# Optimization experiments

Hardware: AMD Instinct MI355X
Metric: run time of the kernel (lower is better)

## Reference

```python
import jax, jax.numpy as jnp
import numpy as np

B, S, D, H = 8, 1024, 1024, 16
DH = D // H


def setup_inputs() -> dict:
    key = jax.random.key(0)
    ks = jax.random.split(key, 8)
    x = jax.random.normal(ks[0], (B, S, D), dtype=jnp.float32)
    # Whisper-style additive causal mask: -inf above the diagonal
    mask = jnp.triu(jnp.full((S, S), -jnp.inf, dtype=jnp.float32), k=1)
    s = 0.02
    Wq = jax.random.normal(ks[1], (D, D), jnp.float32) * s
    bq = jax.random.normal(ks[2], (D,), jnp.float32) * s
    Wk = jax.random.normal(ks[3], (D, D), jnp.float32) * s
    Wv = jax.random.normal(ks[4], (D, D), jnp.float32) * s
    bv = jax.random.normal(ks[5], (D,), jnp.float32) * s
    Wo = jax.random.normal(ks[6], (D, D), jnp.float32) * s
    bo = jax.random.normal(ks[7], (D,), jnp.float32) * s
    return {"x": x, "mask": mask, "Wq": Wq, "bq": bq, "Wk": Wk, "Wv": Wv,
            "bv": bv, "Wo": Wo, "bo": bo}


def reference(x, mask, Wq, bq, Wk, Wv, bv, Wo, bo):
    n_head = H
    d_head = D // n_head
    scale = d_head ** -0.25

    # Projections (torch Linear: y = x @ W.T + b; key has no bias)
    q = x @ Wq.T + bq           # [B,S,D]
    k = x @ Wk.T                # [B,S,D]
    v = x @ Wv.T + bv           # [B,S,D]

    # [B,S,D] -> [B,H,S,dh]
    q = q.reshape(B, S, n_head, d_head).transpose(0, 2, 1, 3)
    k = k.reshape(B, S, n_head, d_head).transpose(0, 2, 1, 3)
    v = v.reshape(B, S, n_head, d_head).transpose(0, 2, 1, 3)

    # Manual (non-fused) attention, fp32 softmax, as in the torch path
    qk = jnp.einsum('bhqd,bhkd->bhqk', q * scale, k * scale)
    qk = qk + mask[:S, :S]
    qk = qk.astype(jnp.float32)
    w = jax.nn.softmax(qk, axis=-1).astype(q.dtype)
    out = jnp.einsum('bhqk,bhkd->bhqd', w, v)
    out = out.transpose(0, 2, 1, 3).reshape(B, S, D)
    out = out @ Wo.T + bo
    qk = jax.lax.stop_gradient(qk)
    return out, qk
```

## Files before the change

kernel.cpp:

```cpp
#include <hip/hip_runtime.h>
#include <math.h>

constexpr int B_ = 8, S_ = 1024, D_ = 1024, H_ = 16, DH_ = 64;
constexpr float MASK_NEG = -1e30f;

typedef __attribute__((ext_vector_type(8))) short short8;
typedef __attribute__((ext_vector_type(4))) float f32x4;

union S8U { short8 s8; unsigned u[4]; };

__device__ __forceinline__ void split8(float4 a, float4 b, short8* hi, short8* lo) {
  float f[8] = {a.x, a.y, a.z, a.w, b.x, b.y, b.z, b.w};
  S8U h, l;
#pragma unroll
  for (int i = 0; i < 4; ++i) {
    float p = f[2 * i], q = f[2 * i + 1];
    unsigned up = __float_as_uint(p), uq = __float_as_uint(q);
    unsigned hp = up & 0xFFFF0000u, hq = uq & 0xFFFF0000u;
    float lp = p - __uint_as_float(hp);
    float lq = q - __uint_as_float(hq);
    h.u[i] = hq | (hp >> 16);
    l.u[i] = (__float_as_uint(lq) & 0xFFFF0000u) | (__float_as_uint(lp) >> 16);
  }
  *hi = h.s8;
  *lo = l.s8;
}

__device__ __forceinline__ void split1v(float f, short& hi, short& lo) {
  unsigned u = __float_as_uint(f);
  unsigned hb = u & 0xFFFF0000u;
  float l = f - __uint_as_float(hb);
  hi = (short)(hb >> 16);
  lo = (short)(__float_as_uint(l) >> 16);
}

__device__ __forceinline__ unsigned pack_sp(float f) {
  unsigned u = __float_as_uint(f);
  unsigned hb = u & 0xFFFF0000u;
  float lo = f - __uint_as_float(hb);
  return hb | (__float_as_uint(lo) >> 16);
}

__device__ __forceinline__ void unpack8(uint4 a, uint4 b, short8* hi, short8* lo) {
  S8U h, l;
  h.u[0] = (a.y & 0xFFFF0000u) | (a.x >> 16);
  h.u[1] = (a.w & 0xFFFF0000u) | (a.z >> 16);
  h.u[2] = (b.y & 0xFFFF0000u) | (b.x >> 16);
  h.u[3] = (b.w & 0xFFFF0000u) | (b.z >> 16);
  l.u[0] = (a.y << 16) | (a.x & 0xFFFFu);
  l.u[1] = (a.w << 16) | (a.z & 0xFFFFu);
  l.u[2] = (b.y << 16) | (b.x & 0xFFFFu);
  l.u[3] = (b.w << 16) | (b.z & 0xFFFFu);
  *hi = h.s8;
  *lo = l.s8;
}

__global__ __launch_bounds__(256) void split_planes(
    const float* __restrict__ x, short* xh, short* xl,
    const float* __restrict__ w0, short* w0h, short* w0l,
    const float* __restrict__ w1, short* w1h, short* w1l,
    const float* __restrict__ w2, short* w2h, short* w2l,
    const float* __restrict__ w3, short* w3h, short* w3l) {
  const float* src; short *dh, *dl; int n8;
  switch (blockIdx.y) {
    case 0:  src = x;  dh = xh;  dl = xl;  n8 = (B_ * S_ * D_) / 8; break;
    case 1:  src = w0; dh = w0h; dl = w0l; n8 = (D_ * D_) / 8; break;
    case 2:  src = w1; dh = w1h; dl = w1l; n8 = (D_ * D_) / 8; break;
    case 3:  src = w2; dh = w2h; dl = w2l; n8 = (D_ * D_) / 8; break;
    default: src = w3; dh = w3h; dl = w3l; n8 = (D_ * D_) / 8; break;
  }
  for (int i = blockIdx.x * 256 + threadIdx.x; i < n8; i += gridDim.x * 256) {
    float4 a = ((const float4*)src)[2 * i];
    float4 b = ((const float4*)src)[2 * i + 1];
    short8 h, l;
    split8(a, b, &h, &l);
    ((short8*)dh)[i] = h;
    ((short8*)dl)[i] = l;
  }
}

__global__ __launch_bounds__(256) void gemm_planes(
    const short* __restrict__ Ah, const short* __restrict__ Al,
    const short* __restrict__ Wh, const short* __restrict__ Wl,
    const float* __restrict__ bias, float scale, int mode,
    float* __restrict__ C, short* __restrict__ Ch, short* __restrict__ Cl,
    int M, int N, int K) {
  __shared__ __align__(16) short As_h[128][40];
  __shared__ __align__(16) short As_l[128][40];
  __shared__ __align__(16) short Bs_h[128][40];
  __shared__ __align__(16) short Bs_l[128][40];

  const int tid = threadIdx.x;
  const int m0 = blockIdx.y * 128, n0 = blockIdx.x * 128;
  const int wave = tid >> 6, lane = tid & 63;
  const int wm = (wave & 1) * 64, wn = (wave >> 1) * 64;
  const int lm = lane & 15;
  const int koff = (lane >> 4) * 8;

  const int r0 = tid >> 2, r1 = (tid >> 2) + 64;
  const int u0 = (tid & 3) * 8;

  f32x4 acc[4][4];
#pragma unroll
  for (int i = 0; i < 4; ++i)
#pragma unroll
    for (int j = 0; j < 4; ++j) acc[i][j] = (f32x4){0.f, 0.f, 0.f, 0.f};

  for (int k0 = 0; k0 < K; k0 += 32) {
    __syncthreads();
    short8 t0 = *(const short8*)(Ah + (size_t)(m0 + r0) * K + k0 + u0);
    short8 t1 = *(const short8*)(Ah + (size_t)(m0 + r1) * K + k0 + u0);
    short8 t2 = *(const short8*)(Al + (size_t)(m0 + r0) * K + k0 + u0);
    short8 t3 = *(const short8*)(Al + (size_t)(m0 + r1) * K + k0 + u0);
    short8 t4 = *(const short8*)(Wh + (size_t)(n0 + r0) * K + k0 + u0);
    short8 t5 = *(const short8*)(Wh + (size_t)(n0 + r1) * K + k0 + u0);
    short8 t6 = *(const short8*)(Wl + (size_t)(n0 + r0) * K + k0 + u0);
    short8 t7 = *(const short8*)(Wl + (size_t)(n0 + r1) * K + k0 + u0);
    *(short8*)&As_h[r0][u0] = t0;
    *(short8*)&As_h[r1][u0] = t1;
    *(short8*)&As_l[r0][u0] = t2;
    *(short8*)&As_l[r1][u0] = t3;
    *(short8*)&Bs_h[r0][u0] = t4;
    *(short8*)&Bs_h[r1][u0] = t5;
    *(short8*)&Bs_l[r0][u0] = t6;
    *(short8*)&Bs_l[r1][u0] = t7;
    __syncthreads();

    short8 ah[4], al[4], bh[4], bl[4];
#pragma unroll
    for (int i = 0; i < 4; ++i) {
      ah[i] = *(const short8*)&As_h[wm + i * 16 + lm][koff];
      al[i] = *(const short8*)&As_l[wm + i * 16 + lm][koff];
      bh[i] = *(const short8*)&Bs_h[wn + i * 16 + lm][koff];
      bl[i] = *(const short8*)&Bs_l[wn + i * 16 + lm][koff];
    }
#pragma unroll
    for (int i = 0; i < 4; ++i)
#pragma unroll
      for (int j = 0; j < 4; ++j) {
        acc[i][j] = __builtin_amdgcn_mfma_f32_16x16x32_bf16(ah[i], bh[j], acc[i][j], 0, 0, 0);
        acc[i][j] = __builtin_amdgcn_mfma_f32_16x16x32_bf16(ah[i], bl[j], acc[i][j], 0, 0, 0);
        acc[i][j] = __builtin_amdgcn_mfma_f32_16x16x32_bf16(al[i], bh[j], acc[i][j], 0, 0, 0);
      }
  }

  const int crow0 = (lane >> 4) * 4;
  const int ccol = lane & 15;
#pragma unroll
  for (int i = 0; i < 4; ++i) {
    const int m = m0 + wm + i * 16 + crow0;
#pragma unroll
    for (int j = 0; j < 4; ++j) {
      const int n = n0 + wn + j * 16 + ccol;
      const float bv_ = bias ? bias[n] : 0.f;
      if (mode == 0) {
#pragma unroll
        for (int r = 0; r < 4; ++r)
          C[(size_t)(m + r) * N + n] = acc[i][j][r] + bv_;
      } else if (mode == 1) {
#pragma unroll
        for (int r = 0; r < 4; ++r) {
          float v = (acc[i][j][r] + bv_) * scale;
          short hv, lv;
          split1v(v, hv, lv);
          Ch[(size_t)(m + r) * N + n] = hv;
          Cl[(size_t)(m + r) * N + n] = lv;
        }
      } else {
        const int bb = m >> 10, ss = m & 1023;
        short4 hv, lv;
        split1v(acc[i][j][0] + bv_, hv.x, lv.x);
        split1v(acc[i][j][1] + bv_, hv.y, lv.y);
        split1v(acc[i][j][2] + bv_, hv.z, lv.z);
        split1v(acc[i][j][3] + bv_, hv.w, lv.w);
        *(short4*)(Ch + ((size_t)bb * D_ + n) * S_ + ss) = hv;
        *(short4*)(Cl + ((size_t)bb * D_ + n) * S_ + ss) = lv;
      }
    }
  }
}

__global__ __launch_bounds__(256) void attn_fused(
    const short* __restrict__ qsh, const short* __restrict__ qsl,
    const short* __restrict__ ksh, const short* __restrict__ ksl,
    const short* __restrict__ vsh, const short* __restrict__ vsl,
    float* __restrict__ qk, short* __restrict__ oh, short* __restrict__ ol) {
  __shared__ __align__(16) short K_hi[64][72];
  __shared__ __align__(16) short K_lo[64][72];
  __shared__ __align__(16) short V_hi[64][72];
  __shared__ __align__(16) short V_lo[64][72];
  __shared__ __align__(16) unsigned P_p[64][68];

  const int it = blockIdx.x;
  const int bh = blockIdx.y;
  const int b = bh >> 4, h = bh & 15;
  const int tid = threadIdx.x;
  const int wave = tid >> 6, lane = tid & 63;
  const int lm = lane & 15, lg = lane >> 4;
  const int wq = wave * 16;
  const int koff = lg * 8;
  const int crow0 = lg * 4;
  const int sr0 = tid >> 3, sr1 = (tid >> 3) + 32;
  const int sc0 = (tid & 7) * 8;

  short8 qfh[2], qfl[2];
  {
    const size_t qb = ((size_t)(b * S_ + it * 64 + wq + lm)) * D_ + h * DH_;
    qfh[0] = *(const short8*)(qsh + qb + koff);
    qfh[1] = *(const short8*)(qsh + qb + 32 + koff);
    qfl[0] = *(const short8*)(qsl + qb + koff);
    qfl[1] = *(const short8*)(qsl + qb + 32 + koff);
  }

  f32x4 O[4];
#pragma unroll
  for (int i = 0; i < 4; ++i) O[i] = (f32x4){0.f, 0.f, 0.f, 0.f};
  f32x4 mreg = (f32x4){MASK_NEG, MASK_NEG, MASK_NEG, MASK_NEG};
  f32x4 lreg = (f32x4){0.f, 0.f, 0.f, 0.f};

  float* qkrow = qk + ((size_t)bh << 20) + (size_t)it * 64 * S_;

  for (int jt = 0; jt <= it; ++jt) {
    __syncthreads();
    const size_t kb = ((size_t)(b * S_ + jt * 64)) * D_ + h * DH_;
    const size_t vb = ((size_t)(b * D_ + h * DH_)) * S_ + jt * 64;
    short8 a0 = *(const short8*)(ksh + kb + (size_t)sr0 * D_ + sc0);
    short8 a1 = *(const short8*)(ksh + kb + (size_t)sr1 * D_ + sc0);
    short8 a2 = *(const short8*)(ksl + kb + (size_t)sr0 * D_ + sc0);
    short8 a3 = *(const short8*)(ksl + kb + (size_t)sr1 * D_ + sc0);
    short8 a4 = *(const short8*)(vsh + vb + (size_t)sr0 * S_ + sc0);
    short8 a5 = *(const short8*)(vsh + vb + (size_t)sr1 * S_ + sc0);
    short8 a6 = *(const short8*)(vsl + vb + (size_t)sr0 * S_ + sc0);
    short8 a7 = *(const short8*)(vsl + vb + (size_t)sr1 * S_ + sc0);
    *(short8*)&K_hi[sr0][sc0] = a0;
    *(short8*)&K_hi[sr1][sc0] = a1;
    *(short8*)&K_lo[sr0][sc0] = a2;
    *(short8*)&K_lo[sr1][sc0] = a3;
    *(short8*)&V_hi[sr0][sc0] = a4;
    *(short8*)&V_hi[sr1][sc0] = a5;
    *(short8*)&V_lo[sr0][sc0] = a6;
    *(short8*)&V_lo[sr1][sc0] = a7;
    __syncthreads();

    f32x4 sacc[4];
#pragma unroll
    for (int j4 = 0; j4 < 4; ++j4) sacc[j4] = (f32x4){0.f, 0.f, 0.f, 0.f};
#pragma unroll
    for (int kc = 0; kc < 2; ++kc)
#pragma unroll
      for (int j4 = 0; j4 < 4; ++j4) {
        short8 kh = *(const short8*)&K_hi[j4 * 16 + lm][kc * 32 + koff];
        short8 kl = *(const short8*)&K_lo[j4 * 16 + lm][kc * 32 + koff];
        sacc[j4] = __builtin_amdgcn_mfma_f32_16x16x32_bf16(qfh[kc], kh, sacc[j4], 0, 0, 0);
        sacc[j4] = __builtin_amdgcn_mfma_f32_16x16x32_bf16(qfh[kc], kl, sacc[j4], 0, 0, 0);
        sacc[j4] = __builtin_amdgcn_mfma_f32_16x16x32_bf16(qfl[kc], kh, sacc[j4], 0, 0, 0);
      }

    if (jt == it) {
#pragma unroll
      for (int j4 = 0; j4 < 4; ++j4)
#pragma unroll
        for (int r = 0; r < 4; ++r)
          if (j4 * 16 + lm > wq + crow0 + r) sacc[j4][r] = MASK_NEG;
    }

#pragma unroll
    for (int j4 = 0; j4 < 4; ++j4)
#pragma unroll
      for (int r = 0; r < 4; ++r)
        qkrow[(size_t)(wq + crow0 + r) * S_ + jt * 64 + j4 * 16 + lm] = sacc[j4][r];

    f32x4 tmax = sacc[0];
#pragma unroll
    for (int j4 = 1; j4 < 4; ++j4)
#pragma unroll
      for (int r = 0; r < 4; ++r) tmax[r] = fmaxf(tmax[r], sacc[j4][r]);
#pragma unroll
    for (int off = 1; off < 16; off <<= 1)
#pragma unroll
      for (int r = 0; r < 4; ++r) tmax[r] = fmaxf(tmax[r], __shfl_xor(tmax[r], off));

    f32x4 fac, mnew;
#pragma unroll
    for (int r = 0; r < 4; ++r) {
      mnew[r] = fmaxf(mreg[r], tmax[r]);
      fac[r] = __expf(mreg[r] - mnew[r]);
      mreg[r] = mnew[r];
    }
    f32x4 tsum = (f32x4){0.f, 0.f, 0.f, 0.f};
#pragma unroll
    for (int j4 = 0; j4 < 4; ++j4)
#pragma unroll
      for (int r = 0; r < 4; ++r) {
        float pv = __expf(sacc[j4][r] - mnew[r]);
        sacc[j4][r] = pv;
        tsum[r] += pv;
      }
#pragma unroll
    for (int off = 1; off < 16; off <<= 1)
#pragma unroll
      for (int r = 0; r < 4; ++r) tsum[r] += __shfl_xor(tsum[r], off);
#pragma unroll
    for (int r = 0; r < 4; ++r) lreg[r] = lreg[r] * fac[r] + tsum[r];
#pragma unroll
    for (int d4 = 0; d4 < 4; ++d4)
#pragma unroll
      for (int r = 0; r < 4; ++r) O[d4][r] *= fac[r];

#pragma unroll
    for (int j4 = 0; j4 < 4; ++j4)
#pragma unroll
      for (int r = 0; r < 4; ++r)
        P_p[wq + crow0 + r][j4 * 16 + lm] = pack_sp(sacc[j4][r]);
    __syncthreads();

#pragma unroll
    for (int kc = 0; kc < 2; ++kc) {
      const unsigned* pp = &P_p[wq + lm][kc * 32 + koff];
      uint4 a0p = *(const uint4*)pp;
      uint4 a1p = *(const uint4*)(pp + 4);
      short8 ph, pl;
      unpack8(a0p, a1p, &ph, &pl);
#pragma unroll
      for (int d4 = 0; d4 < 4; ++d4) {
        short8 vh = *(const short8*)&V_hi[d4 * 16 + lm][kc * 32 + koff];
        short8 vl = *(const short8*)&V_lo[d4 * 16 + lm][kc * 32 + koff];
        O[d4] = __builtin_amdgcn_mfma_f32_16x16x32_bf16(ph, vh, O[d4], 0, 0, 0);
        O[d4] = __builtin_amdgcn_mfma_f32_16x16x32_bf16(ph, vl, O[d4], 0, 0, 0);
        O[d4] = __builtin_amdgcn_mfma_f32_16x16x32_bf16(pl, vh, O[d4], 0, 0, 0);
      }
    }
  }

  {
    f32x4 inv;
#pragma unroll
    for (int r = 0; r < 4; ++r) inv[r] = 1.f / lreg[r];
    const size_t ob = ((size_t)(b * S_ + it * 64 + wq + crow0)) * D_ + h * DH_;
#pragma unroll
    for (int d4 = 0; d4 < 4; ++d4)
#pragma unroll
      for (int r = 0; r < 4; ++r) {
        float v = O[d4][r] * inv[r];
        short hv, lv;
        split1v(v, hv, lv);
        oh[ob + (size_t)r * D_ + d4 * 16 + lm] = hv;
        ol[ob + (size_t)r * D_ + d4 * 16 + lm] = lv;
      }
  }

  const int fr = tid >> 4, fc = (tid & 15) * 4;
  const float4 nf = make_float4(MASK_NEG, MASK_NEG, MASK_NEG, MASK_NEG);
  for (int jt = it + 1; jt < 16; ++jt) {
#pragma unroll
    for (int p = 0; p < 4; ++p) {
      const int r = p * 16 + fr;
      *(float4*)(qkrow + (size_t)r * S_ + jt * 64 + fc) = nf;
    }
  }
}

extern "C" void kernel_launch(void* const* d_in, const int* in_sizes, int n_in,
                              void* d_out, int out_size, void* d_ws,
                              size_t ws_size, hipStream_t stream) {
  const float* x  = (const float*)d_in[0];
  const float* Wq = (const float*)d_in[2];
  const float* bq = (const float*)d_in[3];
  const float* Wk = (const float*)d_in[4];
  const float* Wv = (const float*)d_in[5];
  const float* bv = (const float*)d_in[6];
  const float* Wo = (const float*)d_in[7];
  const float* bo = (const float*)d_in[8];

  float* out = (float*)d_out;
  float* qk  = (float*)d_out + (size_t)B_ * S_ * D_;

  const size_t NSD = (size_t)B_ * S_ * D_;
  const size_t DD = (size_t)D_ * D_;
  short* p = (short*)d_ws;
  short* qh = p;   p += NSD;
  short* ql = p;   p += NSD;
  short* kh = p;   p += NSD;
  short* kl = p;   p += NSD;
  short* vth = p;  p += NSD;
  short* vtl = p;  p += NSD;
  short* ah = p;   p += NSD;
  short* al = p;   p += NSD;
  short* xh = p;   p += NSD;
  short* xl = p;   p += NSD;
  short* wqh = p;  p += DD;  short* wql = p;  p += DD;
  short* wkh = p;  p += DD;  short* wkl = p;  p += DD;
  short* wvh = p;  p += DD;  short* wvl = p;  p += DD;
  short* woh = p;  p += DD;  short* wol = p;  p += DD;

  split_planes<<<dim3(512, 5), 256, 0, stream>>>(
      x, xh, xl, Wq, wqh, wql, Wk, wkh, wkl, Wv, wvh, wvl, Wo, woh, wol);

  const dim3 gg(D_ / 128, (B_ * S_) / 128);
  gemm_planes<<<gg, 256, 0, stream>>>(xh, xl, wqh, wql, bq, 0.125f, 1,
                                      nullptr, qh, ql, B_ * S_, D_, D_);
  gemm_planes<<<gg, 256, 0, stream>>>(xh, xl, wkh, wkl, nullptr, 1.f, 1,
                                      nullptr, kh, kl, B_ * S_, D_, D_);
  gemm_planes<<<gg, 256, 0, stream>>>(xh, xl, wvh, wvl, bv, 1.f, 2,
                                      nullptr, vth, vtl, B_ * S_, D_, D_);

  attn_fused<<<dim3(16, B_ * H_), 256, 0, stream>>>(qh, ql, kh, kl, vth, vtl,
                                                    qk, ah, al);

  gemm_planes<<<gg, 256, 0, stream>>>(ah, al, woh, wol, bo, 1.f, 0,
                                      out, nullptr, nullptr, B_ * S_, D_, D_);
}
```

Baseline: 1.026 ms.

## Use direct global-to-LDS loads in GEMM and XCD-aware block remapping

Replaces the register-staged global loads and LDS stores in the split-bf16 GEMM with global_load_lds 16-byte direct transfers into unpadded LDS tiles. It also remaps block IDs in both the GEMM and attention kernels so that consecutive logical tiles land on the same XCD, which is meant to improve L2 locality across the MI355X chiplets. Removing the LDS padding may add bank conflicts on the MFMA fragment reads. The attention remap hardcodes 16 query tiles per head.

```diff
diff --git a/kernel.cpp b/kernel.cpp
--- a/kernel.cpp
+++ b/kernel.cpp
@@ -8,6 +8,12 @@
 typedef __attribute__((ext_vector_type(4))) float f32x4;
 
 union S8U { short8 s8; unsigned u[4]; };
+
+__device__ __forceinline__ void gl2lds16(const short* g, short* l) {
+  __builtin_amdgcn_global_load_lds(
+      (const __attribute__((address_space(1))) void*)g,
+      (__attribute__((address_space(3))) void*)l, 16, 0, 0);
+}
 
 __device__ __forceinline__ void split8(float4 a, float4 b, short8* hi, short8* lo) {
   float f[8] = {a.x, a.y, a.z, a.w, b.x, b.y, b.z, b.w};
@@ -85,20 +91,25 @@
     const float* __restrict__ bias, float scale, int mode,
     float* __restrict__ C, short* __restrict__ Ch, short* __restrict__ Cl,
     int M, int N, int K) {
-  __shared__ __align__(16) short As_h[128][40];
-  __shared__ __align__(16) short As_l[128][40];
-  __shared__ __align__(16) short Bs_h[128][40];
-  __shared__ __align__(16) short Bs_l[128][40];
+  __shared__ __align__(16) short As_h[128 * 32];
+  __shared__ __align__(16) short As_l[128 * 32];
+  __shared__ __align__(16) short Bs_h[128 * 32];
+  __shared__ __align__(16) short Bs_l[128 * 32];
 
   const int tid = threadIdx.x;
-  const int m0 = blockIdx.y * 128, n0 = blockIdx.x * 128;
+  int id = blockIdx.y * gridDim.x + blockIdx.x;
+  const int cpx = (gridDim.x * gridDim.y) >> 3;
+  id = (id & 7) * cpx + (id >> 3);
+  const int m0 = (id / gridDim.x) * 128, n0 = (id % gridDim.x) * 128;
+
   const int wave = tid >> 6, lane = tid & 63;
   const int wm = (wave & 1) * 64, wn = (wave >> 1) * 64;
   const int lm = lane & 15;
   const int koff = (lane >> 4) * 8;
 
-  const int r0 = tid >> 2, r1 = (tid >> 2) + 64;
-  const int u0 = (tid & 3) * 8;
+  const int hrow = wave * 32;
+  const int grow = hrow + (lane >> 2);
+  const int gcol = (lane & 3) * 8;
 
   f32x4 acc[4][4];
 #pragma unroll
@@ -108,31 +119,25 @@
 
   for (int k0 = 0; k0 < K; k0 += 32) {
     __syncthreads();
-    short8 t0 = *(const short8*)(Ah + (size_t)(m0 + r0) * K + k0 + u0);
-    short8 t1 = *(const short8*)(Ah + (size_t)(m0 + r1) * K + k0 + u0);
-    short8 t2 = *(const short8*)(Al + (size_t)(m0 + r0) * K + k0 + u0);
-    short8 t3 = *(const short8*)(Al + (size_t)(m0 + r1) * K + k0 + u0);
-    short8 t4 = *(const short8*)(Wh + (size_t)(n0 + r0) * K + k0 + u0);
-    short8 t5 = *(const short8*)(Wh + (size_t)(n0 + r1) * K + k0 + u0);
-    short8 t6 = *(const short8*)(Wl + (size_t)(n0 + r0) * K + k0 + u0);
-    short8 t7 = *(const short8*)(Wl + (size_t)(n0 + r1) * K + k0 + u0);
-    *(short8*)&As_h[r0][u0] = t0;
-    *(short8*)&As_h[r1][u0] = t1;
-    *(short8*)&As_l[r0][u0] = t2;
-    *(short8*)&As_l[r1][u0] = t3;
-    *(short8*)&Bs_h[r0][u0] = t4;
-    *(short8*)&Bs_h[r1][u0] = t5;
-    *(short8*)&Bs_l[r0][u0] = t6;
-    *(short8*)&Bs_l[r1][u0] = t7;
+#pragma unroll
+    for (int half = 0; half < 2; ++half) {
+      const size_t ga = (size_t)(m0 + grow + half * 16) * K + k0 + gcol;
+      const size_t gw = (size_t)(n0 + grow + half * 16) * K + k0 + gcol;
+      const int lb = (hrow + half * 16) * 32;
+      gl2lds16(Ah + ga, As_h + lb);
+      gl2lds16(Al + ga, As_l + lb);
+      gl2lds16(Wh + gw, Bs_h + lb);
+      gl2lds16(Wl + gw, Bs_l + lb);
+    }
     __syncthreads();
 
     short8 ah[4], al[4], bh[4], bl[4];
 #pragma unroll
     for (int i = 0; i < 4; ++i) {
-      ah[i] = *(const short8*)&As_h[wm + i * 16 + lm][koff];
-      al[i] = *(const short8*)&As_l[wm + i * 16 + lm][koff];
-      bh[i] = *(const short8*)&Bs_h[wn + i * 16 + lm][koff];
-      bl[i] = *(const short8*)&Bs_l[wn + i * 16 + lm][koff];
+      ah[i] = *(const short8*)&As_h[(wm + i * 16 + lm) * 32 + koff];
+      al[i] = *(const short8*)&As_l[(wm + i * 16 + lm) * 32 + koff];
+      bh[i] = *(const short8*)&Bs_h[(wn + i * 16 + lm) * 32 + koff];
+      bl[i] = *(const short8*)&Bs_l[(wn + i * 16 + lm) * 32 + koff];
     }
 #pragma unroll
     for (int i = 0; i < 4; ++i)
@@ -191,8 +196,11 @@
   __shared__ __align__(16) short V_lo[64][72];
   __shared__ __align__(16) unsigned P_p[64][68];
 
-  const int it = blockIdx.x;
-  const int bh = blockIdx.y;
+  int id = blockIdx.y * gridDim.x + blockIdx.x;
+  const int cpx = (gridDim.x * gridDim.y) >> 3;
+  id = (id & 7) * cpx + (id >> 3);
+  const int it = id & 15;
+  const int bh = id >> 4;
   const int b = bh >> 4, h = bh & 15;
   const int tid = threadIdx.x;
   const int wave = tid >> 6, lane = tid & 63;
```

Result: faster. 948.6 us (-7.5%).
